# Optimization experiments

Hardware: AMD Instinct MI355X
Metric: run time of the kernel (lower is better)

## Reference

```python
import jax, jax.numpy as jnp
import numpy as np

B, S, D, H = 2, 2048, 1024, 16
HD = D // H  # head dim = 64


def setup_inputs() -> dict:
    key = jax.random.key(0)
    ks = jax.random.split(key, 9)
    std = 0.02
    return {
        "hidden_states": jax.random.normal(ks[0], (B, S, D), jnp.float32),
        "wq": jax.random.normal(ks[1], (D, D), jnp.float32) * std,
        "bq": jnp.zeros((D,), jnp.float32),
        "wk": jax.random.normal(ks[2], (D, D), jnp.float32) * std,
        "bk": jnp.zeros((D,), jnp.float32),
        "wv": jax.random.normal(ks[3], (D, D), jnp.float32) * std,
        "bv": jnp.zeros((D,), jnp.float32),
        "wo": jax.random.normal(ks[4], (D, D), jnp.float32) * std,
        "bo": jnp.zeros((D,), jnp.float32),
    }


def reference(hidden_states, wq, bq, wk, bk, wv, bv, wo, bo):
    b, s, d = hidden_states.shape
    # projections (torch Linear: x @ W.T + b; here weights stored as [in,out]-equivalent transpose)
    q = hidden_states @ wq.T + bq
    k = hidden_states @ wk.T + bk
    v = hidden_states @ wv.T + bv
    # [b, h, s, hd]
    q = q.reshape(b, s, H, HD).transpose(0, 2, 1, 3)
    k = k.reshape(b, s, H, HD).transpose(0, 2, 1, 3)
    v = v.reshape(b, s, H, HD).transpose(0, 2, 1, 3)
    scores = jnp.einsum("bhqd,bhkd->bhqk", q, k) / jnp.sqrt(jnp.float32(HD))
    probs = jax.nn.softmax(scores, axis=-1)  # dropout p=0 (eval)
    ctx = jnp.einsum("bhqk,bhkd->bhqd", probs, v)
    ctx = ctx.transpose(0, 2, 1, 3).reshape(b, s, d)
    return ctx @ wo.T + bo
```

## Files before the change

kernel.cpp:

```cpp
#include <hip/hip_runtime.h>
#include <math.h>
#include <stdint.h>

constexpr int BB  = 2;
constexpr int SS  = 2048;
constexpr int DD  = 1024;
constexpr int HH  = 16;
constexpr int HDD = 64;
constexpr int MM  = BB * SS;

typedef uint16_t u16;
typedef __attribute__((ext_vector_type(4))) float    f32x4;
typedef __attribute__((ext_vector_type(8))) _Float16 f16x8;
typedef __attribute__((ext_vector_type(4))) _Float16 f16x4;
typedef __attribute__((ext_vector_type(8))) short    s16x8;
typedef __attribute__((ext_vector_type(4))) short    s16x4;

__device__ __forceinline__ u16 to_f16(float f) {
    const _Float16 h = (_Float16)f;
    return __builtin_bit_cast(u16, h);
}

__device__ __forceinline__ f32x4 mfma32(s16x8 a, s16x8 b, f32x4 c) {
    return __builtin_amdgcn_mfma_f32_16x16x32_f16(
        __builtin_bit_cast(f16x8, a), __builtin_bit_cast(f16x8, b), c, 0, 0, 0);
}
__device__ __forceinline__ f32x4 mfma16(s16x4 a, f16x4 b, f32x4 c) {
    return __builtin_amdgcn_mfma_f32_16x16x16f16(
        __builtin_bit_cast(f16x4, a), b, c, 0, 0, 0);
}

__device__ __forceinline__ void load_lds16(const void* g, void* l) {
    __builtin_amdgcn_global_load_lds(
        (const __attribute__((address_space(1))) void*)g,
        (__attribute__((address_space(3))) void*)l, 16, 0, 0);
}

__global__ __launch_bounds__(256) void cast_x_kernel(
    const float* __restrict__ in, u16* __restrict__ out)
{
    const int i = blockIdx.x * 256 + threadIdx.x;
    const float4* in4 = (const float4*)in;
    const float4 a = in4[i * 2], b = in4[i * 2 + 1];
    s16x8 v;
    v[0] = (short)to_f16(a.x); v[1] = (short)to_f16(a.y);
    v[2] = (short)to_f16(a.z); v[3] = (short)to_f16(a.w);
    v[4] = (short)to_f16(b.x); v[5] = (short)to_f16(b.y);
    v[6] = (short)to_f16(b.z); v[7] = (short)to_f16(b.w);
    *(s16x8*)(out + (size_t)i * 8) = v;
}

__global__ __launch_bounds__(256) void cast_w_kernel(
    const float* __restrict__ w0, const float* __restrict__ w1,
    const float* __restrict__ w2, const float* __restrict__ w3,
    u16* __restrict__ out)
{
    const int i = blockIdx.x * 256 + threadIdx.x;
    const int which = i >> 17;
    const int off   = (i & 131071) * 8;
    const float* w = (which == 0) ? w0 : (which == 1) ? w1 : (which == 2) ? w2 : w3;
    const float4* in4 = (const float4*)(w + off);
    const float4 a = in4[0], b = in4[1];
    s16x8 v;
    v[0] = (short)to_f16(a.x); v[1] = (short)to_f16(a.y);
    v[2] = (short)to_f16(a.z); v[3] = (short)to_f16(a.w);
    v[4] = (short)to_f16(b.x); v[5] = (short)to_f16(b.y);
    v[6] = (short)to_f16(b.z); v[7] = (short)to_f16(b.w);
    *(s16x8*)(out + (size_t)i * 8) = v;
}

template <int MODE>
__global__ __launch_bounds__(256) void gemm_mfma(
    const u16* __restrict__ A, const u16* __restrict__ Wb,
    const float* __restrict__ b0, const float* __restrict__ b1,
    const float* __restrict__ b2,
    float* __restrict__ outf, u16* __restrict__ outq, u16* __restrict__ outv,
    const int K)
{
    __shared__ u16 As[128 * 32];
    __shared__ u16 Bs[128 * 32];

    const int tid = threadIdx.x, lane = tid & 63, wid = tid >> 6;
    const int bm = blockIdx.y * 128;
    const int nb = blockIdx.x * 128;
    const int which = nb >> 10;
    const int ncol  = nb & 1023;
    const u16* Wblk = Wb + ((size_t)which << 20) + (size_t)ncol * K;

    const int srow = lane >> 2;
    const int lu   = (lane & 3) ^ (srow & 3);
    const u16* Ag = A    + (size_t)(bm + srow) * K + lu * 8;
    const u16* Wg = Wblk + (size_t)srow       * K + lu * 8;
    const int c0 = wid * 2, c1 = c0 + 1;

    f32x4 acc[4][4];
#pragma unroll
    for (int i = 0; i < 4; ++i)
#pragma unroll
        for (int j = 0; j < 4; ++j) { f32x4 z = {0.f, 0.f, 0.f, 0.f}; acc[i][j] = z; }

    const int wm = (wid >> 1) * 64, wn = (wid & 1) * 64;

    for (int k0 = 0; k0 < K; k0 += 32) {
        __syncthreads();
        load_lds16(Ag + (size_t)c0 * 16 * K + k0, As + c0 * 512);
        load_lds16(Ag + (size_t)c1 * 16 * K + k0, As + c1 * 512);
        load_lds16(Wg + (size_t)c0 * 16 * K + k0, Bs + c0 * 512);
        load_lds16(Wg + (size_t)c1 * 16 * K + k0, Bs + c1 * 512);
        __syncthreads();

        s16x8 af[4], bf4[4];
#pragma unroll
        for (int i = 0; i < 4; ++i) {
            const int row = wm + i * 16 + (lane & 15);
            const int u   = (lane >> 4) ^ (row & 3);
            af[i] = *(const s16x8*)(As + (size_t)row * 32 + u * 8);
        }
#pragma unroll
        for (int j = 0; j < 4; ++j) {
            const int row = wn + j * 16 + (lane & 15);
            const int u   = (lane >> 4) ^ (row & 3);
            bf4[j] = *(const s16x8*)(Bs + (size_t)row * 32 + u * 8);
        }
#pragma unroll
        for (int i = 0; i < 4; ++i)
#pragma unroll
            for (int j = 0; j < 4; ++j)
                acc[i][j] = mfma32(af[i], bf4[j], acc[i][j]);
    }

    if (MODE == 0) {
#pragma unroll
        for (int j = 0; j < 4; ++j) {
            const int n = nb + wn + j * 16 + (lane & 15);
            const float bb = b0[n];
#pragma unroll
            for (int i = 0; i < 4; ++i) {
                const int m0 = bm + wm + i * 16 + (lane >> 4) * 4;
#pragma unroll
                for (int r = 0; r < 4; ++r)
                    outf[(size_t)(m0 + r) * 1024 + n] = acc[i][j][r] + bb;
            }
        }
    } else {
        const float* bias = (which == 0) ? b0 : (which == 1) ? b1 : b2;
        u16* outb = outq + ((size_t)which << 22);
#pragma unroll
        for (int j = 0; j < 4; ++j) {
            const int nl = ncol + wn + j * 16 + (lane & 15);
            const float bb = bias[nl];
            const int h = nl >> 6, hd = nl & 63;
#pragma unroll
            for (int i = 0; i < 4; ++i) {
                const int m0 = bm + wm + i * 16 + (lane >> 4) * 4;
#pragma unroll
                for (int r = 0; r < 4; ++r) {
                    const int m = m0 + r, b_ = m >> 11, s = m & 2047;
                    const u16 val = to_f16(acc[i][j][r] + bb);
                    if (which < 2) {
                        outb[(((size_t)(b_ * HH + h)) * SS + s) * HDD + hd] = val;
                    } else {
                        const int kt = s >> 6, kv = s & 63;
                        const int g = (kv >> 2) & 3, ii = kv & 3, jj = kv >> 4;
                        const int p = g * 16 + (jj >> 1) * 8 + (jj & 1) * 4 + ii;
                        outv[(((size_t)(b_ * HH + h)) * HDD + hd) * SS + kt * 64 + p] = val;
                    }
                }
            }
        }
    }
}

__global__ __launch_bounds__(256) void attn_mfma(
    const u16* __restrict__ Q, const u16* __restrict__ Kg,
    const u16* __restrict__ Vt, u16* __restrict__ ctx)
{
    __shared__ u16 Ks[64 * 64];
    __shared__ u16 Vs[64 * 64];

    const int tid = threadIdx.x, lane = tid & 63, wid = tid >> 6;
    const int bh = blockIdx.y, q0 = blockIdx.x * 64;
    const u16* Qb = Q  + (size_t)bh * SS * HDD;
    const u16* Kb = Kg + (size_t)bh * SS * HDD;
    const u16* Vb = Vt + (size_t)bh * HDD * SS;

    s16x8 bq[2];
    {
        const int qr = q0 + wid * 16 + (lane & 15);
        bq[0] = *(const s16x8*)(Qb + (size_t)qr * HDD + (lane >> 4) * 8);
        bq[1] = *(const s16x8*)(Qb + (size_t)qr * HDD + 32 + (lane >> 4) * 8);
    }

    f32x4 o[4];
#pragma unroll
    for (int m = 0; m < 4; ++m) { f32x4 z = {0.f, 0.f, 0.f, 0.f}; o[m] = z; }
    float l = 0.f;

    const int c0 = wid * 2, c1 = c0 + 1;
    const int r0 = (c0 * 64 + lane) >> 3, lu0 = ((lane & 7) ^ (r0 & 7));
    const int r1 = (c1 * 64 + lane) >> 3, lu1 = ((lane & 7) ^ (r1 & 7));

    for (int kt = 0; kt < SS / 64; ++kt) {
        __syncthreads();
        load_lds16(Kb + (size_t)(kt * 64 + r0) * HDD + lu0 * 8, Ks + c0 * 512);
        load_lds16(Kb + (size_t)(kt * 64 + r1) * HDD + lu1 * 8, Ks + c1 * 512);
        load_lds16(Vb + (size_t)r0 * SS + kt * 64 + lu0 * 8, Vs + c0 * 512);
        load_lds16(Vb + (size_t)r1 * SS + kt * 64 + lu1 * 8, Vs + c1 * 512);
        __syncthreads();

        f32x4 S[4];
#pragma unroll
        for (int j = 0; j < 4; ++j) {
            const int row = j * 16 + (lane & 15);
            const int sw = row & 7;
            const s16x8 ak0 = *(const s16x8*)(Ks + (size_t)row * 64 + (((lane >> 4)    ) ^ sw) * 8);
            const s16x8 ak1 = *(const s16x8*)(Ks + (size_t)row * 64 + (((lane >> 4) + 4) ^ sw) * 8);
            f32x4 z = {0.f, 0.f, 0.f, 0.f};
            z = mfma32(ak0, bq[0], z);
            z = mfma32(ak1, bq[1], z);
            S[j] = z;
        }

        float partial = 0.f;
        f16x4 pf[4];
#pragma unroll
        for (int j = 0; j < 4; ++j) {
#pragma unroll
            for (int r = 0; r < 4; ++r) {
                const float p = __expf(S[j][r] * 0.125f);
                partial += p;
                pf[j][r] = (_Float16)p;
            }
        }
        partial += __shfl_xor(partial, 16);
        partial += __shfl_xor(partial, 32);
        l += partial;

#pragma unroll
        for (int m = 0; m < 4; ++m) {
            const int row = m * 16 + (lane & 15);
            const int sw = row & 7;
            const s16x8 v0 = *(const s16x8*)(Vs + (size_t)row * 64 + (((lane >> 4) * 2    ) ^ sw) * 8);
            const s16x8 v1 = *(const s16x8*)(Vs + (size_t)row * 64 + (((lane >> 4) * 2 + 1) ^ sw) * 8);
            const s16x4 a0 = __builtin_shufflevector(v0, v0, 0, 1, 2, 3);
            const s16x4 a1 = __builtin_shufflevector(v0, v0, 4, 5, 6, 7);
            const s16x4 a2 = __builtin_shufflevector(v1, v1, 0, 1, 2, 3);
            const s16x4 a3 = __builtin_shufflevector(v1, v1, 4, 5, 6, 7);
            o[m] = mfma16(a0, pf[0], o[m]);
            o[m] = mfma16(a1, pf[1], o[m]);
            o[m] = mfma16(a2, pf[2], o[m]);
            o[m] = mfma16(a3, pf[3], o[m]);
        }
    }

    const int b_ = bh >> 4, h = bh & 15;
    const float inv = 1.f / l;
    const int s_idx = q0 + wid * 16 + (lane & 15);
    u16* orow = ctx + ((size_t)(b_ * SS + s_idx)) * DD + h * HDD;
#pragma unroll
    for (int m = 0; m < 4; ++m) {
        f16x4 w;
#pragma unroll
        for (int r = 0; r < 4; ++r) w[r] = (_Float16)(o[m][r] * inv);
        *(f16x4*)(orow + m * 16 + (lane >> 4) * 4) = w;
    }
}

extern "C" void kernel_launch(void* const* d_in, const int* in_sizes, int n_in,
                              void* d_out, int out_size, void* d_ws, size_t ws_size,
                              hipStream_t stream)
{
    const float* x  = (const float*)d_in[0];
    const float* wq = (const float*)d_in[1];
    const float* bq = (const float*)d_in[2];
    const float* wk = (const float*)d_in[3];
    const float* bk = (const float*)d_in[4];
    const float* wv = (const float*)d_in[5];
    const float* bv = (const float*)d_in[6];
    const float* wo = (const float*)d_in[7];
    const float* bo = (const float*)d_in[8];

    u16* xb   = (u16*)d_ws;
    u16* wb   = xb  + ((size_t)4  << 20);
    u16* qk   = wb  + ((size_t)4  << 20);
    u16* vtw  = qk  + ((size_t)8  << 20);
    u16* ctxb = vtw + ((size_t)4  << 20);

    cast_x_kernel<<<2048, 256, 0, stream>>>(x, xb);
    cast_w_kernel<<<2048, 256, 0, stream>>>(wq, wk, wv, wo, wb);

    gemm_mfma<1><<<dim3(24, 32), 256, 0, stream>>>(
        xb, wb, bq, bk, bv, nullptr, qk, vtw, DD);

    attn_mfma<<<dim3(32, 32), 256, 0, stream>>>(
        qk, qk + ((size_t)4 << 20), vtw, ctxb);

    gemm_mfma<0><<<dim3(8, 32), 256, 0, stream>>>(
        ctxb, wb + ((size_t)3 << 20), bo, nullptr, nullptr,
        (float*)d_out, nullptr, nullptr, DD);
}
```

Measured before the change: 222.7 us.

## Double-buffer attention K/V tiles, use 16x16x32 MFMA for PV, vectorize GEMM epilogues

The attention kernel now keeps two K/V LDS buffers and issues the next tile's async global-to-LDS loads before computing on the current tile, so each iteration needs one barrier instead of two. The P·V product uses the 16x16x32 f16 MFMA on full 8-element fragments instead of four 16x16x16 ops, and the V-transpose layout written by the projection GEMM is changed to match. The GEMMs swap MFMA operand order for the Q/K and output paths so that each lane holds four contiguous columns, allowing 4-wide vector stores with float4 bias loads instead of scalar scatter stores. The two cast kernels are merged into a single launch. The single-barrier double buffer relies on the async LDS loads having completed by the next barrier, and it doubles attention LDS use.

```diff
diff --git a/kernel.cpp b/kernel.cpp
--- a/kernel.cpp
+++ b/kernel.cpp
@@ -14,7 +14,6 @@
 typedef __attribute__((ext_vector_type(8))) _Float16 f16x8;
 typedef __attribute__((ext_vector_type(4))) _Float16 f16x4;
 typedef __attribute__((ext_vector_type(8))) short    s16x8;
-typedef __attribute__((ext_vector_type(4))) short    s16x4;
 
 __device__ __forceinline__ u16 to_f16(float f) {
     const _Float16 h = (_Float16)f;
@@ -25,9 +24,9 @@
     return __builtin_amdgcn_mfma_f32_16x16x32_f16(
         __builtin_bit_cast(f16x8, a), __builtin_bit_cast(f16x8, b), c, 0, 0, 0);
 }
-__device__ __forceinline__ f32x4 mfma16(s16x4 a, f16x4 b, f32x4 c) {
-    return __builtin_amdgcn_mfma_f32_16x16x16f16(
-        __builtin_bit_cast(f16x4, a), b, c, 0, 0, 0);
+__device__ __forceinline__ f32x4 mfma32_ff(s16x8 a, f16x8 b, f32x4 c) {
+    return __builtin_amdgcn_mfma_f32_16x16x32_f16(
+        __builtin_bit_cast(f16x8, a), b, c, 0, 0, 0);
 }
 
 __device__ __forceinline__ void load_lds16(const void* g, void* l) {
@@ -36,37 +35,65 @@
         (__attribute__((address_space(3))) void*)l, 16, 0, 0);
 }
 
-__global__ __launch_bounds__(256) void cast_x_kernel(
-    const float* __restrict__ in, u16* __restrict__ out)
-{
-    const int i = blockIdx.x * 256 + threadIdx.x;
-    const float4* in4 = (const float4*)in;
-    const float4 a = in4[i * 2], b = in4[i * 2 + 1];
+__global__ __launch_bounds__(256) void cast_all(
+    const float* __restrict__ x,
+    const float* __restrict__ w0, const float* __restrict__ w1,
+    const float* __restrict__ w2, const float* __restrict__ w3,
+    u16* __restrict__ xb, u16* __restrict__ wb)
+{
+    const int blk = blockIdx.x, tid = threadIdx.x;
+    const float* src; u16* dst; int idx;
+    if (blk < 2048) { src = x; dst = xb; idx = blk * 256 + tid; }
+    else {
+        const int b2 = blk - 2048, which = b2 >> 9;
+        src = (which == 0) ? w0 : (which == 1) ? w1 : (which == 2) ? w2 : w3;
+        dst = wb + ((size_t)which << 20);
+        idx = (b2 & 511) * 256 + tid;
+    }
+    const float4* in4 = (const float4*)src;
+    const float4 a = in4[idx * 2], b = in4[idx * 2 + 1];
     s16x8 v;
     v[0] = (short)to_f16(a.x); v[1] = (short)to_f16(a.y);
     v[2] = (short)to_f16(a.z); v[3] = (short)to_f16(a.w);
     v[4] = (short)to_f16(b.x); v[5] = (short)to_f16(b.y);
     v[6] = (short)to_f16(b.z); v[7] = (short)to_f16(b.w);
-    *(s16x8*)(out + (size_t)i * 8) = v;
-}
-
-__global__ __launch_bounds__(256) void cast_w_kernel(
-    const float* __restrict__ w0, const float* __restrict__ w1,
-    const float* __restrict__ w2, const float* __restrict__ w3,
-    u16* __restrict__ out)
-{
-    const int i = blockIdx.x * 256 + threadIdx.x;
-    const int which = i >> 17;
-    const int off   = (i & 131071) * 8;
-    const float* w = (which == 0) ? w0 : (which == 1) ? w1 : (which == 2) ? w2 : w3;
-    const float4* in4 = (const float4*)(w + off);
-    const float4 a = in4[0], b = in4[1];
-    s16x8 v;
-    v[0] = (short)to_f16(a.x); v[1] = (short)to_f16(a.y);
-    v[2] = (short)to_f16(a.z); v[3] = (short)to_f16(a.w);
-    v[4] = (short)to_f16(b.x); v[5] = (short)to_f16(b.y);
-    v[6] = (short)to_f16(b.z); v[7] = (short)to_f16(b.w);
-    *(s16x8*)(out + (size_t)i * 8) = v;
+    *(s16x8*)(dst + (size_t)idx * 8) = v;
+}
+
+template <bool SWAP>
+__device__ __forceinline__ void kloop(
+    const u16* __restrict__ Ag, const u16* __restrict__ Wg,
+    u16* As, u16* Bs, const int K, const int c0, const int c1,
+    const int lane, const int wm, const int wn, f32x4 (&acc)[4][4])
+{
+    for (int k0 = 0; k0 < K; k0 += 32) {
+        __syncthreads();
+        load_lds16(Ag + (size_t)c0 * 16 * K + k0, As + c0 * 512);
+        load_lds16(Ag + (size_t)c1 * 16 * K + k0, As + c1 * 512);
+        load_lds16(Wg + (size_t)c0 * 16 * K + k0, Bs + c0 * 512);
+        load_lds16(Wg + (size_t)c1 * 16 * K + k0, Bs + c1 * 512);
+        __syncthreads();
+
+        s16x8 af[4], bf4[4];
+#pragma unroll
+        for (int i = 0; i < 4; ++i) {
+            const int row = wm + i * 16 + (lane & 15);
+            const int u   = (lane >> 4) ^ (row & 3);
+            af[i] = *(const s16x8*)(As + (size_t)row * 32 + u * 8);
+        }
+#pragma unroll
+        for (int j = 0; j < 4; ++j) {
+            const int row = wn + j * 16 + (lane & 15);
+            const int u   = (lane >> 4) ^ (row & 3);
+            bf4[j] = *(const s16x8*)(Bs + (size_t)row * 32 + u * 8);
+        }
+#pragma unroll
+        for (int i = 0; i < 4; ++i)
+#pragma unroll
+            for (int j = 0; j < 4; ++j)
+                acc[i][j] = SWAP ? mfma32(bf4[j], af[i], acc[i][j])
+                                 : mfma32(af[i], bf4[j], acc[i][j]);
+    }
 }
 
 template <int MODE>
@@ -81,6 +108,7 @@
     __shared__ u16 Bs[128 * 32];
 
     const int tid = threadIdx.x, lane = tid & 63, wid = tid >> 6;
+    const int quad = lane >> 4;
     const int bm = blockIdx.y * 128;
     const int nb = blockIdx.x * 128;
     const int which = nb >> 10;
@@ -100,72 +128,62 @@
         for (int j = 0; j < 4; ++j) { f32x4 z = {0.f, 0.f, 0.f, 0.f}; acc[i][j] = z; }
 
     const int wm = (wid >> 1) * 64, wn = (wid & 1) * 64;
-
-    for (int k0 = 0; k0 < K; k0 += 32) {
-        __syncthreads();
-        load_lds16(Ag + (size_t)c0 * 16 * K + k0, As + c0 * 512);
-        load_lds16(Ag + (size_t)c1 * 16 * K + k0, As + c1 * 512);
-        load_lds16(Wg + (size_t)c0 * 16 * K + k0, Bs + c0 * 512);
-        load_lds16(Wg + (size_t)c1 * 16 * K + k0, Bs + c1 * 512);
-        __syncthreads();
-
-        s16x8 af[4], bf4[4];
-#pragma unroll
-        for (int i = 0; i < 4; ++i) {
-            const int row = wm + i * 16 + (lane & 15);
-            const int u   = (lane >> 4) ^ (row & 3);
-            af[i] = *(const s16x8*)(As + (size_t)row * 32 + u * 8);
-        }
-#pragma unroll
-        for (int j = 0; j < 4; ++j) {
-            const int row = wn + j * 16 + (lane & 15);
-            const int u   = (lane >> 4) ^ (row & 3);
-            bf4[j] = *(const s16x8*)(Bs + (size_t)row * 32 + u * 8);
-        }
-#pragma unroll
-        for (int i = 0; i < 4; ++i)
-#pragma unroll
-            for (int j = 0; j < 4; ++j)
-                acc[i][j] = mfma32(af[i], bf4[j], acc[i][j]);
-    }
+    const bool swap = (MODE == 0) || (which < 2);
+    if (swap) kloop<true>(Ag, Wg, As, Bs, K, c0, c1, lane, wm, wn, acc);
+    else      kloop<false>(Ag, Wg, As, Bs, K, c0, c1, lane, wm, wn, acc);
 
     if (MODE == 0) {
 #pragma unroll
         for (int j = 0; j < 4; ++j) {
-            const int n = nb + wn + j * 16 + (lane & 15);
-            const float bb = b0[n];
+            const int n0 = nb + wn + 16 * j + quad * 4;
+            const float4 bv = *(const float4*)&b0[n0];
 #pragma unroll
             for (int i = 0; i < 4; ++i) {
-                const int m0 = bm + wm + i * 16 + (lane >> 4) * 4;
-#pragma unroll
-                for (int r = 0; r < 4; ++r)
-                    outf[(size_t)(m0 + r) * 1024 + n] = acc[i][j][r] + bb;
+                const int m = bm + wm + 16 * i + (lane & 15);
+                f32x4 w = acc[i][j];
+                w[0] += bv.x; w[1] += bv.y; w[2] += bv.z; w[3] += bv.w;
+                *(f32x4*)&outf[(size_t)m * 1024 + n0] = w;
             }
         }
+    } else if (which < 2) {
+        const float* bias = which ? b1 : b0;
+        u16* outb = outq + ((size_t)which << 22);
+        const int h = (ncol + wn) >> 6;
+#pragma unroll
+        for (int j = 0; j < 4; ++j) {
+            const int nl0 = ncol + wn + 16 * j + quad * 4;
+            const float4 bv = *(const float4*)&bias[nl0];
+            const int hd0 = 16 * j + quad * 4;
+#pragma unroll
+            for (int i = 0; i < 4; ++i) {
+                const int m = bm + wm + 16 * i + (lane & 15);
+                const int b_ = m >> 11, s = m & 2047;
+                f16x4 w;
+                w[0] = (_Float16)(acc[i][j][0] + bv.x);
+                w[1] = (_Float16)(acc[i][j][1] + bv.y);
+                w[2] = (_Float16)(acc[i][j][2] + bv.z);
+                w[3] = (_Float16)(acc[i][j][3] + bv.w);
+                *(f16x4*)&outb[(((size_t)(b_ * HH + h)) * SS + s) * HDD + hd0] = w;
+            }
+        }
     } else {
-        const float* bias = (which == 0) ? b0 : (which == 1) ? b1 : b2;
-        u16* outb = outq + ((size_t)which << 22);
-#pragma unroll
-        for (int j = 0; j < 4; ++j) {
-            const int nl = ncol + wn + j * 16 + (lane & 15);
-            const float bb = bias[nl];
+        const int kt = ((bm + wm) & 2047) >> 6;
+        const int b_ = (bm + wm) >> 11;
+#pragma unroll
+        for (int j = 0; j < 4; ++j) {
+            const int nl = ncol + wn + 16 * j + (lane & 15);
+            const float bb = b2[nl];
             const int h = nl >> 6, hd = nl & 63;
+            u16* vrow = outv + (((size_t)(b_ * HH + h)) * HDD + hd) * SS + kt * 64;
 #pragma unroll
             for (int i = 0; i < 4; ++i) {
-                const int m0 = bm + wm + i * 16 + (lane >> 4) * 4;
-#pragma unroll
-                for (int r = 0; r < 4; ++r) {
-                    const int m = m0 + r, b_ = m >> 11, s = m & 2047;
-                    const u16 val = to_f16(acc[i][j][r] + bb);
-                    if (which < 2) {
-                        outb[(((size_t)(b_ * HH + h)) * SS + s) * HDD + hd] = val;
-                    } else {
-                        const int kt = s >> 6, kv = s & 63;
-                        const int g = (kv >> 2) & 3, ii = kv & 3, jj = kv >> 4;
-                        const int p = g * 16 + (jj >> 1) * 8 + (jj & 1) * 4 + ii;
-                        outv[(((size_t)(b_ * HH + h)) * HDD + hd) * SS + kt * 64 + p] = val;
-                    }
-                }
+                const int p0 = (i >> 1) * 32 + quad * 8 + (i & 1) * 4;
+                f16x4 w;
+                w[0] = (_Float16)(acc[i][j][0] + bb);
+                w[1] = (_Float16)(acc[i][j][1] + bb);
+                w[2] = (_Float16)(acc[i][j][2] + bb);
+                w[3] = (_Float16)(acc[i][j][3] + bb);
+                *(f16x4*)&vrow[p0] = w;
             }
         }
     }
@@ -175,20 +193,21 @@
     const u16* __restrict__ Q, const u16* __restrict__ Kg,
     const u16* __restrict__ Vt, u16* __restrict__ ctx)
 {
-    __shared__ u16 Ks[64 * 64];
-    __shared__ u16 Vs[64 * 64];
+    __shared__ u16 Ks[2][64 * 64];
+    __shared__ u16 Vs[2][64 * 64];
 
     const int tid = threadIdx.x, lane = tid & 63, wid = tid >> 6;
+    const int quad = lane >> 4;
     const int bh = blockIdx.y, q0 = blockIdx.x * 64;
     const u16* Qb = Q  + (size_t)bh * SS * HDD;
     const u16* Kb = Kg + (size_t)bh * SS * HDD;
     const u16* Vb = Vt + (size_t)bh * HDD * SS;
 
-    s16x8 bq[2];
+    s16x8 bq0, bq1;
     {
         const int qr = q0 + wid * 16 + (lane & 15);
-        bq[0] = *(const s16x8*)(Qb + (size_t)qr * HDD + (lane >> 4) * 8);
-        bq[1] = *(const s16x8*)(Qb + (size_t)qr * HDD + 32 + (lane >> 4) * 8);
+        bq0 = *(const s16x8*)(Qb + (size_t)qr * HDD + quad * 8);
+        bq1 = *(const s16x8*)(Qb + (size_t)qr * HDD + 32 + quad * 8);
     }
 
     f32x4 o[4];
@@ -199,37 +218,53 @@
     const int c0 = wid * 2, c1 = c0 + 1;
     const int r0 = (c0 * 64 + lane) >> 3, lu0 = ((lane & 7) ^ (r0 & 7));
     const int r1 = (c1 * 64 + lane) >> 3, lu1 = ((lane & 7) ^ (r1 & 7));
+    const u16* Ks0 = Kb + (size_t)r0 * HDD + lu0 * 8;
+    const u16* Ks1 = Kb + (size_t)r1 * HDD + lu1 * 8;
+    const u16* Vs0 = Vb + (size_t)r0 * SS + lu0 * 8;
+    const u16* Vs1 = Vb + (size_t)r1 * SS + lu1 * 8;
+
+    load_lds16(Ks0, &Ks[0][c0 * 512]);
+    load_lds16(Ks1, &Ks[0][c1 * 512]);
+    load_lds16(Vs0, &Vs[0][c0 * 512]);
+    load_lds16(Vs1, &Vs[0][c1 * 512]);
 
     for (int kt = 0; kt < SS / 64; ++kt) {
+        const int buf = kt & 1;
         __syncthreads();
-        load_lds16(Kb + (size_t)(kt * 64 + r0) * HDD + lu0 * 8, Ks + c0 * 512);
-        load_lds16(Kb + (size_t)(kt * 64 + r1) * HDD + lu1 * 8, Ks + c1 * 512);
-        load_lds16(Vb + (size_t)r0 * SS + kt * 64 + lu0 * 8, Vs + c0 * 512);
-        load_lds16(Vb + (size_t)r1 * SS + kt * 64 + lu1 * 8, Vs + c1 * 512);
-        __syncthreads();
+
+        if (kt + 1 < SS / 64) {
+            const int nb_ = buf ^ 1;
+            load_lds16(Ks0 + (size_t)(kt + 1) * 64 * HDD, &Ks[nb_][c0 * 512]);
+            load_lds16(Ks1 + (size_t)(kt + 1) * 64 * HDD, &Ks[nb_][c1 * 512]);
+            load_lds16(Vs0 + (kt + 1) * 64, &Vs[nb_][c0 * 512]);
+            load_lds16(Vs1 + (kt + 1) * 64, &Vs[nb_][c1 * 512]);
+        }
+        const u16* Kbuf = Ks[buf];
+        const u16* Vbuf = Vs[buf];
 
         f32x4 S[4];
 #pragma unroll
         for (int j = 0; j < 4; ++j) {
             const int row = j * 16 + (lane & 15);
             const int sw = row & 7;
-            const s16x8 ak0 = *(const s16x8*)(Ks + (size_t)row * 64 + (((lane >> 4)    ) ^ sw) * 8);
-            const s16x8 ak1 = *(const s16x8*)(Ks + (size_t)row * 64 + (((lane >> 4) + 4) ^ sw) * 8);
+            const s16x8 ak0 = *(const s16x8*)(Kbuf + (size_t)row * 64 + ((quad    ) ^ sw) * 8);
+            const s16x8 ak1 = *(const s16x8*)(Kbuf + (size_t)row * 64 + ((quad + 4) ^ sw) * 8);
             f32x4 z = {0.f, 0.f, 0.f, 0.f};
-            z = mfma32(ak0, bq[0], z);
-            z = mfma32(ak1, bq[1], z);
+            z = mfma32(ak0, bq0, z);
+            z = mfma32(ak1, bq1, z);
             S[j] = z;
         }
 
         float partial = 0.f;
-        f16x4 pf[4];
-#pragma unroll
-        for (int j = 0; j < 4; ++j) {
+        f16x8 pb0, pb1;
+#pragma unroll
+        for (int j4 = 0; j4 < 4; ++j4) {
 #pragma unroll
             for (int r = 0; r < 4; ++r) {
-                const float p = __expf(S[j][r] * 0.125f);
+                const float p = __expf(S[j4][r] * 0.125f);
                 partial += p;
-                pf[j][r] = (_Float16)p;
+                if (j4 < 2) pb0[j4 * 4 + r]      = (_Float16)p;
+                else        pb1[(j4 - 2) * 4 + r] = (_Float16)p;
             }
         }
         partial += __shfl_xor(partial, 16);
@@ -240,16 +275,10 @@
         for (int m = 0; m < 4; ++m) {
             const int row = m * 16 + (lane & 15);
             const int sw = row & 7;
-            const s16x8 v0 = *(const s16x8*)(Vs + (size_t)row * 64 + (((lane >> 4) * 2    ) ^ sw) * 8);
-            const s16x8 v1 = *(const s16x8*)(Vs + (size_t)row * 64 + (((lane >> 4) * 2 + 1) ^ sw) * 8);
-            const s16x4 a0 = __builtin_shufflevector(v0, v0, 0, 1, 2, 3);
-            const s16x4 a1 = __builtin_shufflevector(v0, v0, 4, 5, 6, 7);
-            const s16x4 a2 = __builtin_shufflevector(v1, v1, 0, 1, 2, 3);
-            const s16x4 a3 = __builtin_shufflevector(v1, v1, 4, 5, 6, 7);
-            o[m] = mfma16(a0, pf[0], o[m]);
-            o[m] = mfma16(a1, pf[1], o[m]);
-            o[m] = mfma16(a2, pf[2], o[m]);
-            o[m] = mfma16(a3, pf[3], o[m]);
+            const s16x8 v0 = *(const s16x8*)(Vbuf + (size_t)row * 64 + ((quad    ) ^ sw) * 8);
+            const s16x8 v1 = *(const s16x8*)(Vbuf + (size_t)row * 64 + ((quad + 4) ^ sw) * 8);
+            o[m] = mfma32_ff(v0, pb0, o[m]);
+            o[m] = mfma32_ff(v1, pb1, o[m]);
         }
     }
 
@@ -262,7 +291,7 @@
         f16x4 w;
 #pragma unroll
         for (int r = 0; r < 4; ++r) w[r] = (_Float16)(o[m][r] * inv);
-        *(f16x4*)(orow + m * 16 + (lane >> 4) * 4) = w;
+        *(f16x4*)(orow + m * 16 + quad * 4) = w;
     }
 }
 
@@ -286,8 +315,7 @@
     u16* vtw  = qk  + ((size_t)8  << 20);
     u16* ctxb = vtw + ((size_t)4  << 20);
 
-    cast_x_kernel<<<2048, 256, 0, stream>>>(x, xb);
-    cast_w_kernel<<<2048, 256, 0, stream>>>(wq, wk, wv, wo, wb);
+    cast_all<<<4096, 256, 0, stream>>>(x, wq, wk, wv, wo, xb, wb);
 
     gemm_mfma<1><<<dim3(24, 32), 256, 0, stream>>>(
         xb, wb, bq, bk, bv, nullptr, qk, vtw, DD);
```

After: 230.2 us. 3.4% more time.
